# Performance work log

Hardware: AMD Instinct MI355X
Metric: run time of the kernel (lower is better)

## Reference

```python
import jax, jax.numpy as jnp
import numpy as np

N, E, G = 10000, 320000, 256
IN, H, FP, OUT = 128, 256, 5000, 138


def setup_inputs() -> dict:
    key = jax.random.key(0)
    ks = jax.random.split(key, 12)
    x = jax.random.normal(ks[0], (N, IN), dtype=jnp.float32)
    edge_index = jax.random.randint(ks[1], (2, E), 0, N, dtype=jnp.int64)
    batch_index = jnp.sort(jax.random.randint(ks[2], (N,), 0, G, dtype=jnp.int64))
    grover_fp = jax.random.normal(ks[3], (G, FP), dtype=jnp.float32)
    def lin(k, fan_in, fan_out):
        lim = 1.0 / np.sqrt(fan_in)
        return jax.random.uniform(k, (fan_in, fan_out), jnp.float32, -lim, lim)
    W1 = lin(ks[4], IN, H);            b1 = jnp.zeros((H,), jnp.float32)
    W2 = lin(ks[5], H, H);             b2 = jnp.zeros((H,), jnp.float32)
    Wm1 = lin(ks[6], H + FP, H);       bm1 = jnp.zeros((H,), jnp.float32)
    Wm2 = lin(ks[7], H, OUT);          bm2 = jnp.zeros((OUT,), jnp.float32)
    return {"x": x, "edge_index": edge_index, "batch_index": batch_index,
            "grover_fp": grover_fp, "W1": W1, "b1": b1, "W2": W2, "b2": b2,
            "Wm1": Wm1, "bm1": bm1, "Wm2": Wm2, "bm2": bm2}


def reference(x, edge_index, batch_index, grover_fp, W1, b1, W2, b2, Wm1, bm1, Wm2, bm2):
    n = x.shape[0]
    # GCNConv: add self-loops, symmetric degree normalization D^-1/2 (A+I) D^-1/2
    loop = jnp.arange(n, dtype=edge_index.dtype)
    src = jnp.concatenate([edge_index[0], loop])  # [E+N]
    dst = jnp.concatenate([edge_index[1], loop])
    deg = jax.ops.segment_sum(jnp.ones_like(src, dtype=x.dtype), dst, num_segments=n)
    dinv = jax.lax.rsqrt(jnp.maximum(deg, 1.0))
    norm = dinv[src] * dinv[dst]  # [E+N]

    def gcn(h, W, b):
        hw = h @ W                              # [N, H]
        msg = hw[src] * norm[:, None]           # gather + normalize
        return jax.ops.segment_sum(msg, dst, num_segments=n) + b  # scatter-add

    h = jax.nn.relu(gcn(x, W1, b1))
    h = jax.nn.relu(gcn(h, W2, b2))

    # global mean pool over graphs
    sums = jax.ops.segment_sum(h, batch_index, num_segments=G)        # [G, H]
    cnts = jax.ops.segment_sum(jnp.ones((n,), h.dtype), batch_index, num_segments=G)
    gnn_repr = sums / jnp.maximum(cnts, 1.0)[:, None]

    hcat = jnp.concatenate([gnn_repr, grover_fp], axis=-1)  # [G, H+FP]
    # MLP (dropout is identity in eval mode)
    return jax.nn.relu(hcat @ Wm1 + bm1) @ Wm2 + bm2        # [G, OUT]
```

## Files before the change

kernel.cpp:

```cpp
#include <hip/hip_runtime.h>

constexpr int N_NODES = 10000;
constexpr int E_EDGES = 320000;
constexpr int G_GRAPHS = 256;
constexpr int IN_F = 128;
constexpr int H_F = 256;
constexpr int FP_F = 5000;
constexpr int OUT_F = 138;
constexpr int KCAT = H_F + FP_F;
constexpr int KPAD = 5376;
constexpr int KZ = 21;
constexpr int DMAX = 128;

constexpr int ZB = (N_NODES + 255) / 256;
constexpr int PREP_TOT = H_F * IN_F + H_F * H_F + G_GRAPHS * (KPAD - H_F);
constexpr int PB = (PREP_TOT + 255) / 256;
constexpr int HB = (E_EDGES + 255) / 256;
constexpr int WT_TILES = (KPAD / 64) * (H_F / 64);
constexpr int GB = 157 * 4;
constexpr int M1B = (KZ - 1) * 16;
constexpr int AB = N_NODES / 4;

typedef __attribute__((ext_vector_type(8))) short short8;
typedef __attribute__((ext_vector_type(4))) float f32x4;

static __device__ __forceinline__ unsigned short f2bf(float f) {
    union { float f; unsigned u; } a; a.f = f;
    unsigned r = a.u + 0x7fffu + ((a.u >> 16) & 1u);
    return (unsigned short)(r >> 16);
}
static __device__ __forceinline__ float bf2f(unsigned short u) {
    union { unsigned u; float f; } a; a.u = ((unsigned)u) << 16;
    return a.f;
}

template <int K, bool AF32>
__device__ __forceinline__ void gemm_tile(unsigned short* a_lds, unsigned short* w_lds,
                                          const void* __restrict__ Asrc,
                                          const unsigned short* __restrict__ Wt,
                                          unsigned short* __restrict__ C,
                                          int bm0, int bn0, int tid) {
    constexpr int KB = 128;
    const int lane = tid & 63;
    const int wv = tid >> 6;

    f32x4 acc[4] = {};
    const int rA = wv * 16 + (lane & 15);
    const int kq = (lane >> 4) * 8;

    for (int kb = 0; kb < K; kb += KB) {
        for (int c = tid; c < 64 * KB / 8; c += 256) {
            int r = c >> 4;
            int k = (c & 15) * 8;
            int gr = bm0 + r;
            short8 v = {};
            if (gr < N_NODES) {
                if (AF32) {
                    const float* A = (const float*)Asrc;
                    const float* p = A + (size_t)gr * K + kb + k;
                    float4 lo = *reinterpret_cast<const float4*>(p);
                    float4 hi = *reinterpret_cast<const float4*>(p + 4);
                    v[0] = (short)f2bf(lo.x); v[1] = (short)f2bf(lo.y);
                    v[2] = (short)f2bf(lo.z); v[3] = (short)f2bf(lo.w);
                    v[4] = (short)f2bf(hi.x); v[5] = (short)f2bf(hi.y);
                    v[6] = (short)f2bf(hi.z); v[7] = (short)f2bf(hi.w);
                } else {
                    const unsigned short* A = (const unsigned short*)Asrc;
                    v = *reinterpret_cast<const short8*>(A + (size_t)gr * K + kb + k);
                }
            }
            int byte = r * (2 * KB) + ((2 * k) ^ ((r & 7) << 4));
            *reinterpret_cast<short8*>((char*)a_lds + byte) = v;
        }
        for (int c = tid; c < 64 * KB / 8; c += 256) {
            int r = c >> 4;
            int k = (c & 15) * 8;
            short8 v = *reinterpret_cast<const short8*>(Wt + (size_t)(bn0 + r) * K + kb + k);
            int byte = r * (2 * KB) + ((2 * k) ^ ((r & 7) << 4));
            *reinterpret_cast<short8*>((char*)w_lds + byte) = v;
        }
        __syncthreads();
#pragma unroll
        for (int t = 0; t < KB / 32; ++t) {
            const int k0 = t * 32 + kq;
            short8 af = *reinterpret_cast<const short8*>(
                (char*)a_lds + rA * (2 * KB) + ((2 * k0) ^ ((rA & 7) << 4)));
#pragma unroll
            for (int nt = 0; nt < 4; ++nt) {
                const int rW = nt * 16 + (lane & 15);
                short8 bfr = *reinterpret_cast<const short8*>(
                    (char*)w_lds + rW * (2 * KB) + ((2 * k0) ^ ((rW & 7) << 4)));
                acc[nt] = __builtin_amdgcn_mfma_f32_16x16x32_bf16(bfr, af, acc[nt], 0, 0, 0);
            }
        }
        __syncthreads();
    }

    const int row = bm0 + wv * 16 + (lane & 15);
    if (row < N_NODES) {
#pragma unroll
        for (int nt = 0; nt < 4; ++nt) {
            int col = bn0 + nt * 16 + (lane >> 4) * 4;
            ushort4 o;
            o.x = f2bf(acc[nt][0]);
            o.y = f2bf(acc[nt][1]);
            o.z = f2bf(acc[nt][2]);
            o.w = f2bf(acc[nt][3]);
            *reinterpret_cast<ushort4*>(C + (size_t)row * H_F + col) = o;
        }
    }
}

__device__ __forceinline__ void mlp1_tile(unsigned short* a_lds, unsigned short* w_lds,
                                          const unsigned short* __restrict__ hcat,
                                          const unsigned short* __restrict__ Wt,
                                          float* __restrict__ pz,
                                          int bm0, int bn0, int kz0, int tid) {
    constexpr int KB = 128;
    const int lane = tid & 63;
    const int wv = tid >> 6;

    f32x4 acc[4] = {};
    const int rA = wv * 16 + (lane & 15);
    const int kq = (lane >> 4) * 8;

    for (int kb = kz0; kb < kz0 + 256; kb += KB) {
        for (int c = tid; c < 64 * KB / 8; c += 256) {
            int r = c >> 4;
            int k = (c & 15) * 8;
            short8 v = *reinterpret_cast<const short8*>(hcat + (size_t)(bm0 + r) * KPAD + kb + k);
            int byte = r * (2 * KB) + ((2 * k) ^ ((r & 7) << 4));
            *reinterpret_cast<short8*>((char*)a_lds + byte) = v;
        }
        for (int c = tid; c < 64 * KB / 8; c += 256) {
            int r = c >> 4;
            int k = (c & 15) * 8;
            short8 v = *reinterpret_cast<const short8*>(Wt + (size_t)(bn0 + r) * KPAD + kb + k);
            int byte = r * (2 * KB) + ((2 * k) ^ ((r & 7) << 4));
            *reinterpret_cast<short8*>((char*)w_lds + byte) = v;
        }
        __syncthreads();
#pragma unroll
        for (int t = 0; t < KB / 32; ++t) {
            const int k0 = t * 32 + kq;
            short8 af = *reinterpret_cast<const short8*>(
                (char*)a_lds + rA * (2 * KB) + ((2 * k0) ^ ((rA & 7) << 4)));
#pragma unroll
            for (int nt = 0; nt < 4; ++nt) {
                const int rW = nt * 16 + (lane & 15);
                short8 bfr = *reinterpret_cast<const short8*>(
                    (char*)w_lds + rW * (2 * KB) + ((2 * k0) ^ ((rW & 7) << 4)));
                acc[nt] = __builtin_amdgcn_mfma_f32_16x16x32_bf16(bfr, af, acc[nt], 0, 0, 0);
            }
        }
        __syncthreads();
    }

    const int row = bm0 + wv * 16 + (lane & 15);
#pragma unroll
    for (int nt = 0; nt < 4; ++nt) {
        int col = bn0 + nt * 16 + (lane >> 4) * 4;
        float4 o; o.x = acc[nt][0]; o.y = acc[nt][1]; o.z = acc[nt][2]; o.w = acc[nt][3];
        *reinterpret_cast<float4*>(pz + (size_t)row * H_F + col) = o;
    }
}

__device__ __forceinline__ void agg_body(const unsigned short* __restrict__ hw,
                                         const int* __restrict__ cnt,
                                         const int* __restrict__ srcs_pad,
                                         const float* __restrict__ b,
                                         unsigned short* __restrict__ outp,
                                         int node_base, int tid) {
    const int lane = tid & 63;
    const int node = __builtin_amdgcn_readfirstlane(node_base + (tid >> 6));
    const float dd = rsqrtf((float)cnt[node] + 1.0f);
    const unsigned short* rowb = hw + lane * 4;
    const int* sp = srcs_pad + (node << 7);

    float a0, a1, a2, a3;
    {
        const ushort4 sv = *reinterpret_cast<const ushort4*>(hw + (size_t)node * H_F + lane * 4);
        const float4 bv = *reinterpret_cast<const float4*>(b + lane * 4);
        const float ddsq = dd * dd;
        a0 = bf2f(sv.x) * ddsq + bv.x;
        a1 = bf2f(sv.y) * ddsq + bv.y;
        a2 = bf2f(sv.z) * ddsq + bv.z;
        a3 = bf2f(sv.w) * ddsq + bv.w;
    }

    const int e1 = __builtin_amdgcn_readfirstlane(min(cnt[node], DMAX));
    int e = 0;
    for (; e + 8 <= e1; e += 8) {
        ushort4 v[8];
        float w[8];
#pragma unroll
        for (int q = 0; q < 8; ++q) {
            const int s = sp[e + q];
            w[q] = rsqrtf((float)cnt[s] + 1.0f) * dd;
            v[q] = *reinterpret_cast<const ushort4*>(rowb + (size_t)s * H_F);
        }
#pragma unroll
        for (int q = 0; q < 8; ++q) {
            a0 += bf2f(v[q].x) * w[q];
            a1 += bf2f(v[q].y) * w[q];
            a2 += bf2f(v[q].z) * w[q];
            a3 += bf2f(v[q].w) * w[q];
        }
    }
    for (; e < e1; ++e) {
        const int s = sp[e];
        const float w = rsqrtf((float)cnt[s] + 1.0f) * dd;
        const ushort4 v = *reinterpret_cast<const ushort4*>(rowb + (size_t)s * H_F);
        a0 += bf2f(v.x) * w;
        a1 += bf2f(v.y) * w;
        a2 += bf2f(v.z) * w;
        a3 += bf2f(v.w) * w;
    }
    ushort4 o;
    o.x = f2bf(fmaxf(a0, 0.0f));
    o.y = f2bf(fmaxf(a1, 0.0f));
    o.z = f2bf(fmaxf(a2, 0.0f));
    o.w = f2bf(fmaxf(a3, 0.0f));
    *reinterpret_cast<ushort4*>(outp + (size_t)node * H_F + lane * 4) = o;
}

__global__ void k_p1(const float* __restrict__ W1, const float* __restrict__ W2,
                     const float* __restrict__ gfp, int* __restrict__ cnt,
                     unsigned short* __restrict__ W1t, unsigned short* __restrict__ W2t,
                     unsigned short* __restrict__ hcat) {
    const int bx = blockIdx.x;
    if (bx < ZB) {
        int i = bx * 256 + threadIdx.x;
        if (i < N_NODES) cnt[i] = 0;
        return;
    }
    int i = (bx - ZB) * 256 + threadIdx.x;
    if (i < H_F * IN_F) {
        int c = i / IN_F, k = i - c * IN_F;
        W1t[i] = f2bf(W1[(size_t)k * H_F + c]);
        return;
    }
    i -= H_F * IN_F;
    if (i < H_F * H_F) {
        int c = i >> 8, k = i & 255;
        W2t[i] = f2bf(W2[(size_t)k * H_F + c]);
        return;
    }
    i -= H_F * H_F;
    const int W = KPAD - H_F;
    if (i < G_GRAPHS * W) {
        int g = i / W, k = i - g * W;
        hcat[(size_t)g * KPAD + H_F + k] = (k < FP_F) ? f2bf(gfp[(size_t)g * FP_F + k])
                                                      : (unsigned short)0;
    }
}

__global__ __launch_bounds__(256) void k_p2(const float* __restrict__ x,
                                            const unsigned short* __restrict__ W1t,
                                            unsigned short* __restrict__ Abf,
                                            const int* __restrict__ ei,
                                            int* __restrict__ cnt,
                                            int* __restrict__ srcs_pad,
                                            const float* __restrict__ Wm1,
                                            unsigned short* __restrict__ Wt) {
    __shared__ unsigned short a_lds[64 * 128];
    __shared__ unsigned short w_lds[64 * 128];
    int bx = blockIdx.x;
    if (bx < GB) {
        gemm_tile<IN_F, true>(a_lds, w_lds, x, W1t, Abf, (bx % 157) * 64, (bx / 157) * 64,
                              threadIdx.x);
        return;
    }
    bx -= GB;
    if (bx < HB) {
        int e = bx * 256 + threadIdx.x;
        if (e < E_EDGES) {
            int s = ei[e];
            int d = ei[E_EDGES + e];
            int p = atomicAdd(&cnt[d], 1);
            if (p < DMAX) srcs_pad[(d << 7) + p] = s;
        }
        return;
    }
    bx -= HB;
    float* tbuf = (float*)a_lds;
    const int k0 = (bx % (KPAD / 64)) * 64;
    const int c0 = (bx / (KPAD / 64)) * 64;
    for (int idx = threadIdx.x; idx < 64 * 64; idx += 256) {
        int r = idx >> 6, cc = idx & 63;
        int k = k0 + r;
        tbuf[r * 65 + cc] = (k < KCAT) ? Wm1[(size_t)k * H_F + c0 + cc] : 0.0f;
    }
    __syncthreads();
    for (int idx = threadIdx.x; idx < 64 * 64; idx += 256) {
        int r = idx >> 6, kk = idx & 63;
        Wt[(size_t)(c0 + r) * KPAD + k0 + kk] = f2bf(tbuf[kk * 65 + r]);
    }
}

__global__ __launch_bounds__(256) void k_p3(const unsigned short* __restrict__ Abf,
                                            const int* __restrict__ cnt,
                                            const int* __restrict__ srcs_pad,
                                            const float* __restrict__ b1,
                                            unsigned short* __restrict__ h1,
                                            const unsigned short* __restrict__ hcat,
                                            const unsigned short* __restrict__ Wm1t,
                                            float* __restrict__ partial) {
    __shared__ unsigned short a_lds[64 * 128];
    __shared__ unsigned short w_lds[64 * 128];
    int bx = blockIdx.x;
    if (bx < AB) {
        agg_body(Abf, cnt, srcs_pad, b1, h1, bx * 4, threadIdx.x);
        return;
    }
    bx -= AB;
    const int z = bx / 16 + 1;
    const int r = bx % 16;
    mlp1_tile(a_lds, w_lds, hcat, Wm1t, partial + (size_t)(z - 1) * (G_GRAPHS * H_F),
              (r & 3) * 64, (r >> 2) * 64, z * 256, threadIdx.x);
}

__global__ __launch_bounds__(256) void k_p4(const unsigned short* __restrict__ h1,
                                            const unsigned short* __restrict__ W2t,
                                            unsigned short* __restrict__ Abf) {
    __shared__ unsigned short a_lds[64 * 128];
    __shared__ unsigned short w_lds[64 * 128];
    gemm_tile<H_F, false>(a_lds, w_lds, h1, W2t, Abf, (blockIdx.x % 157) * 64,
                          (blockIdx.x / 157) * 64, threadIdx.x);
}

__global__ __launch_bounds__(256) void k_p5(const unsigned short* __restrict__ Abf,
                                            const int* __restrict__ cnt,
                                            const int* __restrict__ srcs_pad,
                                            const float* __restrict__ b2,
                                            unsigned short* __restrict__ h1) {
    agg_body(Abf, cnt, srcs_pad, b2, h1, blockIdx.x * 4, threadIdx.x);
}

__global__ void k_fin(const unsigned short* __restrict__ h1, const int* __restrict__ batch,
                      const unsigned short* __restrict__ Wm1t,
                      const float* __restrict__ partial, const float* __restrict__ bm1,
                      const float* __restrict__ Wm2, const float* __restrict__ bm2,
                      float* __restrict__ out) {
    __shared__ float m[H_F];
    __shared__ float hrow[H_F];
    const int g = blockIdx.x;
    const int j = threadIdx.x;
    int lo = 0, hi = N_NODES;
    while (lo < hi) { int mm = (lo + hi) >> 1; if (batch[mm] < g) lo = mm + 1; else hi = mm; }
    const int s = lo;
    lo = s; hi = N_NODES;
    while (lo < hi) { int mm = (lo + hi) >> 1; if (batch[mm] < g + 1) lo = mm + 1; else hi = mm; }
    const int e = lo;
    float c0 = 0.0f, c1 = 0.0f, c2 = 0.0f, c3 = 0.0f;
    int i = s;
    for (; i + 4 <= e; i += 4) {
        c0 += bf2f(h1[(size_t)(i + 0) * H_F + j]);
        c1 += bf2f(h1[(size_t)(i + 1) * H_F + j]);
        c2 += bf2f(h1[(size_t)(i + 2) * H_F + j]);
        c3 += bf2f(h1[(size_t)(i + 3) * H_F + j]);
    }
    for (; i < e; ++i) c0 += bf2f(h1[(size_t)i * H_F + j]);
    hrow[j] = ((c0 + c1) + (c2 + c3)) / fmaxf((float)(e - s), 1.0f);
    __syncthreads();

    float acc = bm1[j];
    for (int k = 0; k < H_F; k += 8) {
        short8 wv = *reinterpret_cast<const short8*>(Wm1t + (size_t)j * KPAD + k);
#pragma unroll
        for (int q = 0; q < 8; ++q) acc += hrow[k + q] * bf2f((unsigned short)wv[q]);
    }
    for (int z = 0; z < KZ - 1; ++z)
        acc += partial[((size_t)z * G_GRAPHS + g) * H_F + j];
    m[j] = fmaxf(acc, 0.0f);
    __syncthreads();
    if (j < OUT_F) {
        float a = bm2[j];
        for (int k = 0; k < H_F; ++k) a += m[k] * Wm2[k * OUT_F + j];
        out[g * OUT_F + j] = a;
    }
}

extern "C" void kernel_launch(void* const* d_in, const int* in_sizes, int n_in,
                              void* d_out, int out_size, void* d_ws, size_t ws_size,
                              hipStream_t stream) {
    const float* x       = (const float*)d_in[0];
    const int*   ei      = (const int*)d_in[1];
    const int*   batch   = (const int*)d_in[2];
    const float* gfp     = (const float*)d_in[3];
    const float* W1      = (const float*)d_in[4];
    const float* b1      = (const float*)d_in[5];
    const float* W2      = (const float*)d_in[6];
    const float* b2      = (const float*)d_in[7];
    const float* Wm1     = (const float*)d_in[8];
    const float* bm1     = (const float*)d_in[9];
    const float* Wm2     = (const float*)d_in[10];
    const float* bm2     = (const float*)d_in[11];
    float* out = (float*)d_out;

    unsigned short* W1t  = (unsigned short*)d_ws;
    unsigned short* W2t  = W1t + IN_F * H_F;
    unsigned short* Abf  = W2t + H_F * H_F;
    unsigned short* h1   = Abf + (size_t)N_NODES * H_F;
    unsigned short* hcat = h1 + (size_t)N_NODES * H_F;
    unsigned short* Wm1t = hcat + (size_t)G_GRAPHS * KPAD;
    float* partial = (float*)(Wm1t + (size_t)H_F * KPAD);
    int* cnt      = (int*)(partial + (size_t)(KZ - 1) * G_GRAPHS * H_F);
    int* srcs_pad = cnt + N_NODES;

    k_p1<<<ZB + PB, 256, 0, stream>>>(W1, W2, gfp, cnt, W1t, W2t, hcat);

    k_p2<<<GB + HB + WT_TILES, 256, 0, stream>>>(x, W1t, Abf, ei, cnt, srcs_pad, Wm1, Wm1t);

    k_p3<<<AB + M1B, 256, 0, stream>>>(Abf, cnt, srcs_pad, b1, h1, hcat, Wm1t, partial);

    {
        dim3 g2(157 * 4);
        k_p4<<<g2, 256, 0, stream>>>(h1, W2t, Abf);
    }

    k_p5<<<AB, 256, 0, stream>>>(Abf, cnt, srcs_pad, b2, h1);

    k_fin<<<G_GRAPHS, H_F, 0, stream>>>(h1, batch, Wm1t, partial, bm1, Wm2, bm2, out);
}
```

Before: 112.5 us.

## Fuse all phases into one cooperative persistent kernel with grid syncs

Replaces the six separate kernel launches with one cooperative persistent kernel. Each phase is a grid-strided work loop, and phases are separated by grid.sync() calls. It also moves the W2 GEMM into the same phase as the MLP1 split-K tiles, and vectorizes the fingerprint bf16 conversion to 8 elements per thread. The aim is to remove launch overhead and kernel-boundary drains and to overlap independent work. The risk is the cost of grid-wide barriers, plus possible loss of occupancy when only a limited number of resident blocks is launched.

```diff
diff --git a/kernel.cpp b/kernel.cpp
--- a/kernel.cpp
+++ b/kernel.cpp
@@ -1,4 +1,7 @@
 #include <hip/hip_runtime.h>
+#include <hip/hip_cooperative_groups.h>
+
+namespace cg = cooperative_groups;
 
 constexpr int N_NODES = 10000;
 constexpr int E_EDGES = 320000;
@@ -13,16 +16,34 @@
 constexpr int DMAX = 128;
 
 constexpr int ZB = (N_NODES + 255) / 256;
-constexpr int PREP_TOT = H_F * IN_F + H_F * H_F + G_GRAPHS * (KPAD - H_F);
-constexpr int PB = (PREP_TOT + 255) / 256;
+constexpr int W1TB = H_F * IN_F / 256;
+constexpr int W2TB = H_F * H_F / 256;
+constexpr int FPB = G_GRAPHS * (KPAD - H_F) / 8 / 256;
+constexpr int GB = 157 * 4;
 constexpr int HB = (E_EDGES + 255) / 256;
 constexpr int WT_TILES = (KPAD / 64) * (H_F / 64);
-constexpr int GB = 157 * 4;
 constexpr int M1B = (KZ - 1) * 16;
 constexpr int AB = N_NODES / 4;
 
+constexpr int N0 = ZB + W1TB + W2TB + FPB;
+constexpr int N1 = GB + HB + WT_TILES;
+constexpr int N2 = AB;
+constexpr int N3 = GB + M1B;
+constexpr int N4 = AB;
+constexpr int N5 = G_GRAPHS;
+
 typedef __attribute__((ext_vector_type(8))) short short8;
 typedef __attribute__((ext_vector_type(4))) float f32x4;
+
+struct Params {
+    const float* x; const int* ei; const int* batch; const float* gfp;
+    const float* W1; const float* b1; const float* W2; const float* b2;
+    const float* Wm1; const float* bm1; const float* Wm2; const float* bm2;
+    float* out;
+    unsigned short* W1t; unsigned short* W2t; unsigned short* Abf;
+    unsigned short* h1; unsigned short* hcat; unsigned short* Wm1t;
+    float* partial; int* cnt; int* srcs_pad;
+};
 
 static __device__ __forceinline__ unsigned short f2bf(float f) {
     union { float f; unsigned u; } a; a.f = f;
@@ -224,202 +245,213 @@
     *reinterpret_cast<ushort4*>(outp + (size_t)node * H_F + lane * 4) = o;
 }
 
-__global__ void k_p1(const float* __restrict__ W1, const float* __restrict__ W2,
-                     const float* __restrict__ gfp, int* __restrict__ cnt,
-                     unsigned short* __restrict__ W1t, unsigned short* __restrict__ W2t,
-                     unsigned short* __restrict__ hcat) {
-    const int bx = blockIdx.x;
-    if (bx < ZB) {
-        int i = bx * 256 + threadIdx.x;
-        if (i < N_NODES) cnt[i] = 0;
-        return;
-    }
-    int i = (bx - ZB) * 256 + threadIdx.x;
-    if (i < H_F * IN_F) {
-        int c = i / IN_F, k = i - c * IN_F;
-        W1t[i] = f2bf(W1[(size_t)k * H_F + c]);
-        return;
-    }
-    i -= H_F * IN_F;
-    if (i < H_F * H_F) {
+__device__ __forceinline__ void work0(const Params& p, int w, int tid) {
+    if (w < ZB) {
+        int i = w * 256 + tid;
+        if (i < N_NODES) p.cnt[i] = 0;
+        return;
+    }
+    w -= ZB;
+    if (w < W1TB) {
+        int i = w * 256 + tid;
+        int c = i >> 7, k = i & 127;
+        p.W1t[i] = f2bf(p.W1[(size_t)k * H_F + c]);
+        return;
+    }
+    w -= W1TB;
+    if (w < W2TB) {
+        int i = w * 256 + tid;
         int c = i >> 8, k = i & 255;
-        W2t[i] = f2bf(W2[(size_t)k * H_F + c]);
-        return;
-    }
-    i -= H_F * H_F;
-    const int W = KPAD - H_F;
-    if (i < G_GRAPHS * W) {
-        int g = i / W, k = i - g * W;
-        hcat[(size_t)g * KPAD + H_F + k] = (k < FP_F) ? f2bf(gfp[(size_t)g * FP_F + k])
-                                                      : (unsigned short)0;
-    }
-}
-
-__global__ __launch_bounds__(256) void k_p2(const float* __restrict__ x,
-                                            const unsigned short* __restrict__ W1t,
-                                            unsigned short* __restrict__ Abf,
-                                            const int* __restrict__ ei,
-                                            int* __restrict__ cnt,
-                                            int* __restrict__ srcs_pad,
-                                            const float* __restrict__ Wm1,
-                                            unsigned short* __restrict__ Wt) {
-    __shared__ unsigned short a_lds[64 * 128];
-    __shared__ unsigned short w_lds[64 * 128];
-    int bx = blockIdx.x;
-    if (bx < GB) {
-        gemm_tile<IN_F, true>(a_lds, w_lds, x, W1t, Abf, (bx % 157) * 64, (bx / 157) * 64,
-                              threadIdx.x);
-        return;
-    }
-    bx -= GB;
-    if (bx < HB) {
-        int e = bx * 256 + threadIdx.x;
+        p.W2t[i] = f2bf(p.W2[(size_t)k * H_F + c]);
+        return;
+    }
+    w -= W2TB;
+    {
+        int idx = w * 256 + tid;
+        int g = idx / 640, k = (idx - g * 640) * 8;
+        short8 v = {};
+        if (k < FP_F) {
+            const float* src = p.gfp + (size_t)g * FP_F + k;
+            float4 lo = *reinterpret_cast<const float4*>(src);
+            float4 hi = *reinterpret_cast<const float4*>(src + 4);
+            v[0] = (short)f2bf(lo.x); v[1] = (short)f2bf(lo.y);
+            v[2] = (short)f2bf(lo.z); v[3] = (short)f2bf(lo.w);
+            v[4] = (short)f2bf(hi.x); v[5] = (short)f2bf(hi.y);
+            v[6] = (short)f2bf(hi.z); v[7] = (short)f2bf(hi.w);
+        }
+        *reinterpret_cast<short8*>(p.hcat + (size_t)g * KPAD + H_F + k) = v;
+    }
+}
+
+__device__ __forceinline__ void work1(const Params& p, int w, int tid,
+                                      unsigned short* a_lds, unsigned short* w_lds) {
+    if (w < GB) {
+        gemm_tile<IN_F, true>(a_lds, w_lds, p.x, p.W1t, p.Abf, (w % 157) * 64, (w / 157) * 64,
+                              tid);
+        return;
+    }
+    w -= GB;
+    if (w < HB) {
+        int e = w * 256 + tid;
         if (e < E_EDGES) {
-            int s = ei[e];
-            int d = ei[E_EDGES + e];
-            int p = atomicAdd(&cnt[d], 1);
-            if (p < DMAX) srcs_pad[(d << 7) + p] = s;
-        }
-        return;
-    }
-    bx -= HB;
+            int s = p.ei[e];
+            int d = p.ei[E_EDGES + e];
+            int pos = atomicAdd(&p.cnt[d], 1);
+            if (pos < DMAX) p.srcs_pad[(d << 7) + pos] = s;
+        }
+        return;
+    }
+    w -= HB;
     float* tbuf = (float*)a_lds;
-    const int k0 = (bx % (KPAD / 64)) * 64;
-    const int c0 = (bx / (KPAD / 64)) * 64;
-    for (int idx = threadIdx.x; idx < 64 * 64; idx += 256) {
+    const int k0 = (w % (KPAD / 64)) * 64;
+    const int c0 = (w / (KPAD / 64)) * 64;
+    for (int idx = tid; idx < 64 * 64; idx += 256) {
         int r = idx >> 6, cc = idx & 63;
         int k = k0 + r;
-        tbuf[r * 65 + cc] = (k < KCAT) ? Wm1[(size_t)k * H_F + c0 + cc] : 0.0f;
+        tbuf[r * 65 + cc] = (k < KCAT) ? p.Wm1[(size_t)k * H_F + c0 + cc] : 0.0f;
     }
     __syncthreads();
-    for (int idx = threadIdx.x; idx < 64 * 64; idx += 256) {
+    for (int idx = tid; idx < 64 * 64; idx += 256) {
         int r = idx >> 6, kk = idx & 63;
-        Wt[(size_t)(c0 + r) * KPAD + k0 + kk] = f2bf(tbuf[kk * 65 + r]);
-    }
-}
-
-__global__ __launch_bounds__(256) void k_p3(const unsigned short* __restrict__ Abf,
-                                            const int* __restrict__ cnt,
-                                            const int* __restrict__ srcs_pad,
-                                            const float* __restrict__ b1,
-                                            unsigned short* __restrict__ h1,
-                                            const unsigned short* __restrict__ hcat,
-                                            const unsigned short* __restrict__ Wm1t,
-                                            float* __restrict__ partial) {
-    __shared__ unsigned short a_lds[64 * 128];
-    __shared__ unsigned short w_lds[64 * 128];
-    int bx = blockIdx.x;
-    if (bx < AB) {
-        agg_body(Abf, cnt, srcs_pad, b1, h1, bx * 4, threadIdx.x);
-        return;
-    }
-    bx -= AB;
-    const int z = bx / 16 + 1;
-    const int r = bx % 16;
-    mlp1_tile(a_lds, w_lds, hcat, Wm1t, partial + (size_t)(z - 1) * (G_GRAPHS * H_F),
-              (r & 3) * 64, (r >> 2) * 64, z * 256, threadIdx.x);
-}
-
-__global__ __launch_bounds__(256) void k_p4(const unsigned short* __restrict__ h1,
-                                            const unsigned short* __restrict__ W2t,
-                                            unsigned short* __restrict__ Abf) {
-    __shared__ unsigned short a_lds[64 * 128];
-    __shared__ unsigned short w_lds[64 * 128];
-    gemm_tile<H_F, false>(a_lds, w_lds, h1, W2t, Abf, (blockIdx.x % 157) * 64,
-                          (blockIdx.x / 157) * 64, threadIdx.x);
-}
-
-__global__ __launch_bounds__(256) void k_p5(const unsigned short* __restrict__ Abf,
-                                            const int* __restrict__ cnt,
-                                            const int* __restrict__ srcs_pad,
-                                            const float* __restrict__ b2,
-                                            unsigned short* __restrict__ h1) {
-    agg_body(Abf, cnt, srcs_pad, b2, h1, blockIdx.x * 4, threadIdx.x);
-}
-
-__global__ void k_fin(const unsigned short* __restrict__ h1, const int* __restrict__ batch,
-                      const unsigned short* __restrict__ Wm1t,
-                      const float* __restrict__ partial, const float* __restrict__ bm1,
-                      const float* __restrict__ Wm2, const float* __restrict__ bm2,
-                      float* __restrict__ out) {
-    __shared__ float m[H_F];
-    __shared__ float hrow[H_F];
-    const int g = blockIdx.x;
-    const int j = threadIdx.x;
+        p.Wm1t[(size_t)(c0 + r) * KPAD + k0 + kk] = f2bf(tbuf[kk * 65 + r]);
+    }
+    __syncthreads();
+}
+
+__device__ __forceinline__ void work3(const Params& p, int w, int tid,
+                                      unsigned short* a_lds, unsigned short* w_lds) {
+    if (w < GB) {
+        gemm_tile<H_F, false>(a_lds, w_lds, p.h1, p.W2t, p.Abf, (w % 157) * 64,
+                              (w / 157) * 64, tid);
+        return;
+    }
+    w -= GB;
+    const int z = w / 16 + 1;
+    const int r = w % 16;
+    mlp1_tile(a_lds, w_lds, p.hcat, p.Wm1t, p.partial + (size_t)(z - 1) * (G_GRAPHS * H_F),
+              (r & 3) * 64, (r >> 2) * 64, z * 256, tid);
+}
+
+__device__ __forceinline__ void work5(const Params& p, int g, int tid,
+                                      unsigned short* a_lds, unsigned short* w_lds) {
+    float* hrow = (float*)a_lds;
+    float* m = (float*)w_lds;
+    const int j = tid;
     int lo = 0, hi = N_NODES;
-    while (lo < hi) { int mm = (lo + hi) >> 1; if (batch[mm] < g) lo = mm + 1; else hi = mm; }
+    while (lo < hi) { int mm = (lo + hi) >> 1; if (p.batch[mm] < g) lo = mm + 1; else hi = mm; }
     const int s = lo;
     lo = s; hi = N_NODES;
-    while (lo < hi) { int mm = (lo + hi) >> 1; if (batch[mm] < g + 1) lo = mm + 1; else hi = mm; }
+    while (lo < hi) { int mm = (lo + hi) >> 1; if (p.batch[mm] < g + 1) lo = mm + 1; else hi = mm; }
     const int e = lo;
     float c0 = 0.0f, c1 = 0.0f, c2 = 0.0f, c3 = 0.0f;
     int i = s;
     for (; i + 4 <= e; i += 4) {
-        c0 += bf2f(h1[(size_t)(i + 0) * H_F + j]);
-        c1 += bf2f(h1[(size_t)(i + 1) * H_F + j]);
-        c2 += bf2f(h1[(size_t)(i + 2) * H_F + j]);
-        c3 += bf2f(h1[(size_t)(i + 3) * H_F + j]);
-    }
-    for (; i < e; ++i) c0 += bf2f(h1[(size_t)i * H_F + j]);
+        c0 += bf2f(p.h1[(size_t)(i + 0) * H_F + j]);
+        c1 += bf2f(p.h1[(size_t)(i + 1) * H_F + j]);
+        c2 += bf2f(p.h1[(size_t)(i + 2) * H_F + j]);
+        c3 += bf2f(p.h1[(size_t)(i + 3) * H_F + j]);
+    }
+    for (; i < e; ++i) c0 += bf2f(p.h1[(size_t)i * H_F + j]);
     hrow[j] = ((c0 + c1) + (c2 + c3)) / fmaxf((float)(e - s), 1.0f);
     __syncthreads();
 
-    float acc = bm1[j];
+    float acc = p.bm1[j];
     for (int k = 0; k < H_F; k += 8) {
-        short8 wv = *reinterpret_cast<const short8*>(Wm1t + (size_t)j * KPAD + k);
+        short8 wv = *reinterpret_cast<const short8*>(p.Wm1t + (size_t)j * KPAD + k);
 #pragma unroll
         for (int q = 0; q < 8; ++q) acc += hrow[k + q] * bf2f((unsigned short)wv[q]);
     }
     for (int z = 0; z < KZ - 1; ++z)
-        acc += partial[((size_t)z * G_GRAPHS + g) * H_F + j];
+        acc += p.partial[((size_t)z * G_GRAPHS + g) * H_F + j];
     m[j] = fmaxf(acc, 0.0f);
     __syncthreads();
     if (j < OUT_F) {
-        float a = bm2[j];
-        for (int k = 0; k < H_F; ++k) a += m[k] * Wm2[k * OUT_F + j];
-        out[g * OUT_F + j] = a;
+        float a = p.bm2[j];
+        for (int k = 0; k < H_F; ++k) a += m[k] * p.Wm2[k * OUT_F + j];
+        p.out[g * OUT_F + j] = a;
+    }
+    __syncthreads();
+}
+
+__global__ __launch_bounds__(256) void mega(Params p) {
+    __shared__ unsigned short a_lds[64 * 128];
+    __shared__ unsigned short w_lds[64 * 128];
+    cg::grid_group grid = cg::this_grid();
+    const int tid = threadIdx.x;
+    const int nb = gridDim.x;
+
+    for (int w = blockIdx.x; w < N0; w += nb) work0(p, w, tid);
+    grid.sync();
+    for (int w = blockIdx.x; w < N1; w += nb) work1(p, w, tid, a_lds, w_lds);
+    grid.sync();
+    for (int w = blockIdx.x; w < N2; w += nb) agg_body(p.Abf, p.cnt, p.srcs_pad, p.b1, p.h1, w * 4, tid);
+    grid.sync();
+    for (int w = blockIdx.x; w < N3; w += nb) work3(p, w, tid, a_lds, w_lds);
+    grid.sync();
+    for (int w = blockIdx.x; w < N4; w += nb) agg_body(p.Abf, p.cnt, p.srcs_pad, p.b2, p.h1, w * 4, tid);
+    grid.sync();
+    for (int w = blockIdx.x; w < N5; w += nb) work5(p, w, tid, a_lds, w_lds);
+}
+
+__global__ __launch_bounds__(256) void k_phase(Params p, int ph) {
+    __shared__ unsigned short a_lds[64 * 128];
+    __shared__ unsigned short w_lds[64 * 128];
+    const int tid = threadIdx.x;
+    const int w = blockIdx.x;
+    switch (ph) {
+        case 0: work0(p, w, tid); break;
+        case 1: work1(p, w, tid, a_lds, w_lds); break;
+        case 2: agg_body(p.Abf, p.cnt, p.srcs_pad, p.b1, p.h1, w * 4, tid); break;
+        case 3: work3(p, w, tid, a_lds, w_lds); break;
+        case 4: agg_body(p.Abf, p.cnt, p.srcs_pad, p.b2, p.h1, w * 4, tid); break;
+        case 5: work5(p, w, tid, a_lds, w_lds); break;
     }
 }
 
 extern "C" void kernel_launch(void* const* d_in, const int* in_sizes, int n_in,
                               void* d_out, int out_size, void* d_ws, size_t ws_size,
                               hipStream_t stream) {
-    const float* x       = (const float*)d_in[0];
-    const int*   ei      = (const int*)d_in[1];
-    const int*   batch   = (const int*)d_in[2];
-    const float* gfp     = (const float*)d_in[3];
-    const float* W1      = (const float*)d_in[4];
-    const float* b1      = (const float*)d_in[5];
-    const float* W2      = (const float*)d_in[6];
-    const float* b2      = (const float*)d_in[7];
-    const float* Wm1     = (const float*)d_in[8];
-    const float* bm1     = (const float*)d_in[9];
-    const float* Wm2     = (const float*)d_in[10];
-    const float* bm2     = (const float*)d_in[11];
-    float* out = (float*)d_out;
-
-    unsigned short* W1t  = (unsigned short*)d_ws;
-    unsigned short* W2t  = W1t + IN_F * H_F;
-    unsigned short* Abf  = W2t + H_F * H_F;
-    unsigned short* h1   = Abf + (size_t)N_NODES * H_F;
-    unsigned short* hcat = h1 + (size_t)N_NODES * H_F;
-    unsigned short* Wm1t = hcat + (size_t)G_GRAPHS * KPAD;
-    float* partial = (float*)(Wm1t + (size_t)H_F * KPAD);
-    int* cnt      = (int*)(partial + (size_t)(KZ - 1) * G_GRAPHS * H_F);
-    int* srcs_pad = cnt + N_NODES;
-
-    k_p1<<<ZB + PB, 256, 0, stream>>>(W1, W2, gfp, cnt, W1t, W2t, hcat);
-
-    k_p2<<<GB + HB + WT_TILES, 256, 0, stream>>>(x, W1t, Abf, ei, cnt, srcs_pad, Wm1, Wm1t);
-
-    k_p3<<<AB + M1B, 256, 0, stream>>>(Abf, cnt, srcs_pad, b1, h1, hcat, Wm1t, partial);
-
-    {
-        dim3 g2(157 * 4);
-        k_p4<<<g2, 256, 0, stream>>>(h1, W2t, Abf);
-    }
-
-    k_p5<<<AB, 256, 0, stream>>>(Abf, cnt, srcs_pad, b2, h1);
-
-    k_fin<<<G_GRAPHS, H_F, 0, stream>>>(h1, batch, Wm1t, partial, bm1, Wm2, bm2, out);
-}
+    Params p;
+    p.x    = (const float*)d_in[0];
+    p.ei   = (const int*)d_in[1];
+    p.batch= (const int*)d_in[2];
+    p.gfp  = (const float*)d_in[3];
+    p.W1   = (const float*)d_in[4];
+    p.b1   = (const float*)d_in[5];
+    p.W2   = (const float*)d_in[6];
+    p.b2   = (const float*)d_in[7];
+    p.Wm1  = (const float*)d_in[8];
+    p.bm1  = (const float*)d_in[9];
+    p.Wm2  = (const float*)d_in[10];
+    p.bm2  = (const float*)d_in[11];
+    p.out  = (float*)d_out;
+
+    p.W1t  = (unsigned short*)d_ws;
+    p.W2t  = p.W1t + IN_F * H_F;
+    p.Abf  = p.W2t + H_F * H_F;
+    p.h1   = p.Abf + (size_t)N_NODES * H_F;
+    p.hcat = p.h1 + (size_t)N_NODES * H_F;
+    p.Wm1t = p.hcat + (size_t)G_GRAPHS * KPAD;
+    p.partial = (float*)(p.Wm1t + (size_t)H_F * KPAD);
+    p.cnt  = (int*)(p.partial + (size_t)(KZ - 1) * G_GRAPHS * H_F);
+    p.srcs_pad = p.cnt + N_NODES;
+
+    int occ = 0;
+    if (hipOccupancyMaxActiveBlocksPerMultiprocessor(&occ, (const void*)mega, 256, 0) !=
+            hipSuccess || occ <= 0)
+        occ = 4;
+    if (occ > 5) occ = 5;
+    int nblk = occ * 256;
+
+    void* kargs[] = { (void*)&p };
+    hipError_t le = hipLaunchCooperativeKernel((const void*)mega, dim3(nblk), dim3(256),
+                                               kargs, 0, stream);
+    if (le != hipSuccess) {
+        k_phase<<<N0, 256, 0, stream>>>(p, 0);
+        k_phase<<<N1, 256, 0, stream>>>(p, 1);
+        k_phase<<<N2, 256, 0, stream>>>(p, 2);
+        k_phase<<<N3, 256, 0, stream>>>(p, 3);
+        k_phase<<<N4, 256, 0, stream>>>(p, 4);
+        k_phase<<<N5, 256, 0, stream>>>(p, 5);
+    }
+}
```

New measurement: 341.9 us. 204% more time.

## Split MLP1 K-chunks across two aggregation kernels and vectorize fingerprint conversion

Applied to the files above, without the earlier changes.

The MLP1 split-K partial GEMM tiles used to run alongside only the first aggregation kernel. They are now split in half: chunks 1–10 stay with k_p3 and chunks 11–20 move into k_p5, so both aggregation passes carry some GEMM work to overlap. The prep kernel is also restructured into per-section block ranges, and the grover_fp to bf16 conversion now uses float4 loads and 8-wide stores. This adds LDS use to k_p5, which may lower its occupancy for the memory-bound aggregation.

```diff
diff --git a/kernel.cpp b/kernel.cpp
--- a/kernel.cpp
+++ b/kernel.cpp
@@ -13,12 +13,13 @@
 constexpr int DMAX = 128;
 
 constexpr int ZB = (N_NODES + 255) / 256;
-constexpr int PREP_TOT = H_F * IN_F + H_F * H_F + G_GRAPHS * (KPAD - H_F);
-constexpr int PB = (PREP_TOT + 255) / 256;
+constexpr int W1TB = H_F * IN_F / 256;
+constexpr int W2TB = H_F * H_F / 256;
+constexpr int FPB = G_GRAPHS * (KPAD - H_F) / 8 / 256;
 constexpr int HB = (E_EDGES + 255) / 256;
 constexpr int WT_TILES = (KPAD / 64) * (H_F / 64);
 constexpr int GB = 157 * 4;
-constexpr int M1B = (KZ - 1) * 16;
+constexpr int M1H = 160;
 constexpr int AB = N_NODES / 4;
 
 typedef __attribute__((ext_vector_type(8))) short short8;
@@ -228,30 +229,41 @@
                      const float* __restrict__ gfp, int* __restrict__ cnt,
                      unsigned short* __restrict__ W1t, unsigned short* __restrict__ W2t,
                      unsigned short* __restrict__ hcat) {
-    const int bx = blockIdx.x;
-    if (bx < ZB) {
-        int i = bx * 256 + threadIdx.x;
+    int w = blockIdx.x;
+    if (w < ZB) {
+        int i = w * 256 + threadIdx.x;
         if (i < N_NODES) cnt[i] = 0;
         return;
     }
-    int i = (bx - ZB) * 256 + threadIdx.x;
-    if (i < H_F * IN_F) {
-        int c = i / IN_F, k = i - c * IN_F;
+    w -= ZB;
+    if (w < W1TB) {
+        int i = w * 256 + threadIdx.x;
+        int c = i >> 7, k = i & 127;
         W1t[i] = f2bf(W1[(size_t)k * H_F + c]);
         return;
     }
-    i -= H_F * IN_F;
-    if (i < H_F * H_F) {
+    w -= W1TB;
+    if (w < W2TB) {
+        int i = w * 256 + threadIdx.x;
         int c = i >> 8, k = i & 255;
         W2t[i] = f2bf(W2[(size_t)k * H_F + c]);
         return;
     }
-    i -= H_F * H_F;
-    const int W = KPAD - H_F;
-    if (i < G_GRAPHS * W) {
-        int g = i / W, k = i - g * W;
-        hcat[(size_t)g * KPAD + H_F + k] = (k < FP_F) ? f2bf(gfp[(size_t)g * FP_F + k])
-                                                      : (unsigned short)0;
+    w -= W2TB;
+    {
+        int idx = w * 256 + threadIdx.x;
+        int g = idx / 640, k = (idx - g * 640) * 8;
+        short8 v = {};
+        if (k < FP_F) {
+            const float* src = gfp + (size_t)g * FP_F + k;
+            float4 lo = *reinterpret_cast<const float4*>(src);
+            float4 hi = *reinterpret_cast<const float4*>(src + 4);
+            v[0] = (short)f2bf(lo.x); v[1] = (short)f2bf(lo.y);
+            v[2] = (short)f2bf(lo.z); v[3] = (short)f2bf(lo.w);
+            v[4] = (short)f2bf(hi.x); v[5] = (short)f2bf(hi.y);
+            v[6] = (short)f2bf(hi.z); v[7] = (short)f2bf(hi.w);
+        }
+        *reinterpret_cast<short8*>(hcat + (size_t)g * KPAD + H_F + k) = v;
     }
 }
 
@@ -333,8 +345,22 @@
                                             const int* __restrict__ cnt,
                                             const int* __restrict__ srcs_pad,
                                             const float* __restrict__ b2,
-                                            unsigned short* __restrict__ h1) {
-    agg_body(Abf, cnt, srcs_pad, b2, h1, blockIdx.x * 4, threadIdx.x);
+                                            unsigned short* __restrict__ h1,
+                                            const unsigned short* __restrict__ hcat,
+                                            const unsigned short* __restrict__ Wm1t,
+                                            float* __restrict__ partial) {
+    __shared__ unsigned short a_lds[64 * 128];
+    __shared__ unsigned short w_lds[64 * 128];
+    int bx = blockIdx.x;
+    if (bx < AB) {
+        agg_body(Abf, cnt, srcs_pad, b2, h1, bx * 4, threadIdx.x);
+        return;
+    }
+    bx -= AB;
+    const int z = bx / 16 + 11;
+    const int r = bx % 16;
+    mlp1_tile(a_lds, w_lds, hcat, Wm1t, partial + (size_t)(z - 1) * (G_GRAPHS * H_F),
+              (r & 3) * 64, (r >> 2) * 64, z * 256, threadIdx.x);
 }
 
 __global__ void k_fin(const unsigned short* __restrict__ h1, const int* __restrict__ batch,
@@ -408,18 +434,15 @@
     int* cnt      = (int*)(partial + (size_t)(KZ - 1) * G_GRAPHS * H_F);
     int* srcs_pad = cnt + N_NODES;
 
-    k_p1<<<ZB + PB, 256, 0, stream>>>(W1, W2, gfp, cnt, W1t, W2t, hcat);
+    k_p1<<<ZB + W1TB + W2TB + FPB, 256, 0, stream>>>(W1, W2, gfp, cnt, W1t, W2t, hcat);
 
     k_p2<<<GB + HB + WT_TILES, 256, 0, stream>>>(x, W1t, Abf, ei, cnt, srcs_pad, Wm1, Wm1t);
 
-    k_p3<<<AB + M1B, 256, 0, stream>>>(Abf, cnt, srcs_pad, b1, h1, hcat, Wm1t, partial);
-
-    {
-        dim3 g2(157 * 4);
-        k_p4<<<g2, 256, 0, stream>>>(h1, W2t, Abf);
-    }
-
-    k_p5<<<AB, 256, 0, stream>>>(Abf, cnt, srcs_pad, b2, h1);
+    k_p3<<<AB + M1H, 256, 0, stream>>>(Abf, cnt, srcs_pad, b1, h1, hcat, Wm1t, partial);
+
+    k_p4<<<GB, 256, 0, stream>>>(h1, W2t, Abf);
+
+    k_p5<<<AB + M1H, 256, 0, stream>>>(Abf, cnt, srcs_pad, b2, h1, hcat, Wm1t, partial);
 
     k_fin<<<G_GRAPHS, H_F, 0, stream>>>(h1, batch, Wm1t, partial, bm1, Wm2, bm2, out);
 }
```

Measured after the change: 117.8 us. +4.8%, slower.
